# Kernel optimization log

Measured on AMD Instinct MI355X. Metric: run time of the kernel, lower is better.

## Reference

```python
import jax, jax.numpy as jnp
import numpy as np

B, T, C = 1, 4096, 1024
NH, NKV, HD = 16, 4, 64
N_REP = NH // NKV
WIN = 1024
EPS = 1e-5
ROPE_THETA = 10000.0


def setup_inputs() -> dict:
    key = jax.random.key(0)
    ks = jax.random.split(key, 6)
    s = 1.0 / np.sqrt(C)
    x = jax.random.normal(ks[0], (B, T, C), jnp.float32)
    wq = jax.random.normal(ks[1], (NH * HD, C), jnp.float32) * s
    wk = jax.random.normal(ks[2], (NKV * HD, C), jnp.float32) * s
    wv = jax.random.normal(ks[3], (NKV * HD, C), jnp.float32) * s
    wo = jax.random.normal(ks[4], (C, NH * HD), jnp.float32) * (1.0 / np.sqrt(NH * HD))
    q_norm_w = jnp.ones((HD,), jnp.float32)
    k_norm_w = jnp.ones((HD,), jnp.float32)
    # RoPE tables: (T, HD//2)
    inv_freq = 1.0 / (ROPE_THETA ** (np.arange(0, HD, 2, dtype=np.float32) / HD))
    ang = np.outer(np.arange(T, dtype=np.float32), inv_freq)
    freqs_cos = jnp.asarray(np.cos(ang), jnp.float32)
    freqs_sin = jnp.asarray(np.sin(ang), jnp.float32)
    return {"x": x, "wq": wq, "wk": wk, "wv": wv, "wo": wo,
            "q_norm_w": q_norm_w, "k_norm_w": k_norm_w,
            "freqs_cos": freqs_cos, "freqs_sin": freqs_sin}


def _rmsnorm(v, w):
    # RMSNorm over last dim (per-head)
    return v * jax.lax.rsqrt(jnp.mean(v * v, axis=-1, keepdims=True) + EPS) * w


def _rope(v, cos, sin):
    # v: (B, T, H, HD); interleaved complex rotation, matching torch polar freqs_cis
    vr, vi = v[..., 0::2], v[..., 1::2]
    c = cos[None, :, None, :]
    s = sin[None, :, None, :]
    out_r = vr * c - vi * s
    out_i = vr * s + vi * c
    return jnp.stack([out_r, out_i], axis=-1).reshape(v.shape)


def reference(x, wq, wk, wv, wo, q_norm_w, k_norm_w, freqs_cos, freqs_sin):
    xq = jnp.einsum('btc,dc->btd', x, wq).reshape(B, T, NH, HD)
    xk = jnp.einsum('btc,dc->btd', x, wk).reshape(B, T, NKV, HD)
    xv = jnp.einsum('btc,dc->btd', x, wv).reshape(B, T, NKV, HD)
    # per-head QK RMSNorm
    xq = _rmsnorm(xq, q_norm_w)
    xk = _rmsnorm(xk, k_norm_w)
    # RoPE
    xq = _rope(xq, freqs_cos, freqs_sin)
    xk = _rope(xk, freqs_cos, freqs_sin)
    # GQA: expand kv heads
    xk = jnp.repeat(xk, N_REP, axis=2)  # (B, T, NH, HD)
    xv = jnp.repeat(xv, N_REP, axis=2)
    scale = 1.0 / np.sqrt(HD)
    scores = jnp.einsum('bthd,bshd->bhts', xq, xk) * scale
    i = jnp.arange(T)[:, None]
    j = jnp.arange(T)[None, :]
    mask = (i >= j) & (i - j < WIN)  # causal + sliding window
    scores = jnp.where(mask[None, None], scores, -jnp.inf)
    attn = jax.nn.softmax(scores, axis=-1)
    y = jnp.einsum('bhts,bshd->bthd', attn, xv).reshape(B, T, NH * HD)
    return jnp.einsum('btd,cd->btc', y, wo)
```

## Files before the change

### kernel.cpp

```cpp
#include <hip/hip_runtime.h>
#include <hip/hip_bf16.h>


#define WIN_SZ 1024

typedef __attribute__((ext_vector_type(8))) short short8;
typedef __attribute__((ext_vector_type(8))) unsigned short ushort8;
typedef __attribute__((ext_vector_type(4))) float f32x4;
typedef __attribute__((ext_vector_type(16))) float f32x16;

__device__ __forceinline__ unsigned short f2bf(float f) {
  union { float f; unsigned u; } v; v.f = f;
  unsigned r = v.u + 0x7fffu + ((v.u >> 16) & 1u);
  return (unsigned short)(r >> 16);
}

__device__ __forceinline__ float bf2f(unsigned short b) {
  union { unsigned u; float f; } v; v.u = ((unsigned)b) << 16; return v.f;
}

__device__ __forceinline__ unsigned pk2bf(float lo, float hi) {
  __hip_bfloat162 h = __float22bfloat162_rn(make_float2(lo, hi));
  union { __hip_bfloat162 h; unsigned u; } c; c.h = h; return c.u;
}

__device__ __forceinline__ short8 frag4(unsigned w0, unsigned w1, unsigned w2, unsigned w3) {
  union { unsigned u[4]; short8 s; } x;
  x.u[0] = w0; x.u[1] = w1; x.u[2] = w2; x.u[3] = w3; return x.s;
}

__device__ __forceinline__ ushort8 pack8(float4 a, float4 b) {
  union { unsigned u[4]; ushort8 s; } x;
  x.u[0] = pk2bf(a.x, a.y); x.u[1] = pk2bf(a.z, a.w);
  x.u[2] = pk2bf(b.x, b.y); x.u[3] = pk2bf(b.z, b.w);
  return x.s;
}

__global__ __launch_bounds__(256) void k_gemm_qkv(const float* __restrict__ x,
                                                  const float* __restrict__ wq,
                                                  const float* __restrict__ wk,
                                                  const float* __restrict__ wv,
                                                  unsigned short* __restrict__ C) {
  __shared__ unsigned short As[128 * 64];
  __shared__ unsigned short Bs[128 * 64];
  char* Asb = (char*)As;
  char* Bsb = (char*)Bs;
  const int tid = threadIdx.x;
  const int w = tid >> 6, l = tid & 63;
  const int wr = w >> 1, wc = w & 1;
  const int r = l & 15, g = l >> 4;
  const int m0 = blockIdx.y * 128, n0 = blockIdx.x * 128;
  const int crow = tid >> 3, cslot = tid & 7;

  const float* Bp;
  if (n0 < 1024) Bp = wq + (size_t)n0 * 1024;
  else if (n0 < 1280) Bp = wk + (size_t)(n0 - 1024) * 1024;
  else Bp = wv + (size_t)(n0 - 1280) * 1024;

  f32x4 acc[4][4];
#pragma unroll
  for (int i = 0; i < 4; i++)
#pragma unroll
    for (int j = 0; j < 4; j++) acc[i][j] = {0.f, 0.f, 0.f, 0.f};

  for (int k0 = 0; k0 < 1024; k0 += 64) {
#pragma unroll
    for (int i = 0; i < 4; i++) {
      int row = crow + i * 32;
      int dst = row * 128 + ((cslot * 16) ^ ((row & 7) << 4));
      const float4* ap = (const float4*)(x + (size_t)(m0 + row) * 1024 + k0 + cslot * 8);
      *(ushort8*)(Asb + dst) = pack8(ap[0], ap[1]);
      const float4* bp = (const float4*)(Bp + (size_t)row * 1024 + k0 + cslot * 8);
      *(ushort8*)(Bsb + dst) = pack8(bp[0], bp[1]);
    }
    __syncthreads();
#pragma unroll
    for (int kk = 0; kk < 2; kk++) {
      short8 af[4], bfr[4];
#pragma unroll
      for (int mi = 0; mi < 4; mi++) {
        int row = wr * 64 + mi * 16 + r;
        af[mi] = *(const short8*)(Asb + row * 128 + ((kk * 64 + g * 16) ^ ((row & 7) << 4)));
      }
#pragma unroll
      for (int nj = 0; nj < 4; nj++) {
        int row = wc * 64 + nj * 16 + r;
        bfr[nj] = *(const short8*)(Bsb + row * 128 + ((kk * 64 + g * 16) ^ ((row & 7) << 4)));
      }
#pragma unroll
      for (int mi = 0; mi < 4; mi++)
#pragma unroll
        for (int nj = 0; nj < 4; nj++)
          acc[mi][nj] = __builtin_amdgcn_mfma_f32_16x16x32_bf16(af[mi], bfr[nj], acc[mi][nj], 0, 0, 0);
    }
    __syncthreads();
  }

#pragma unroll
  for (int mi = 0; mi < 4; mi++)
#pragma unroll
    for (int nj = 0; nj < 4; nj++) {
      int row = m0 + wr * 64 + mi * 16 + g * 4;
      int col = n0 + wc * 64 + nj * 16 + r;
#pragma unroll
      for (int e = 0; e < 4; e++)
        C[(size_t)(row + e) * 1536 + col] = f2bf(acc[mi][nj][e]);
    }
}

__global__ __launch_bounds__(256) void k_gemm_out(const unsigned short* __restrict__ A,
                                                  const float* __restrict__ wo,
                                                  float* __restrict__ C) {
  __shared__ unsigned short As[128 * 64];
  __shared__ unsigned short Bs[128 * 64];
  char* Asb = (char*)As;
  char* Bsb = (char*)Bs;
  const int tid = threadIdx.x;
  const int w = tid >> 6, l = tid & 63;
  const int wr = w >> 1, wc = w & 1;
  const int r = l & 15, g = l >> 4;
  const int m0 = blockIdx.y * 128, n0 = blockIdx.x * 128;
  const int crow = tid >> 3, cslot = tid & 7;

  f32x4 acc[4][4];
#pragma unroll
  for (int i = 0; i < 4; i++)
#pragma unroll
    for (int j = 0; j < 4; j++) acc[i][j] = {0.f, 0.f, 0.f, 0.f};

  for (int k0 = 0; k0 < 1024; k0 += 64) {
#pragma unroll
    for (int i = 0; i < 4; i++) {
      int row = crow + i * 32;
      int dst = row * 128 + ((cslot * 16) ^ ((row & 7) << 4));
      ushort8 va = *(const ushort8*)(A + (size_t)(m0 + row) * 1024 + k0 + cslot * 8);
      *(ushort8*)(Asb + dst) = va;
      const float4* bp = (const float4*)(wo + (size_t)(n0 + row) * 1024 + k0 + cslot * 8);
      *(ushort8*)(Bsb + dst) = pack8(bp[0], bp[1]);
    }
    __syncthreads();
#pragma unroll
    for (int kk = 0; kk < 2; kk++) {
      short8 af[4], bfr[4];
#pragma unroll
      for (int mi = 0; mi < 4; mi++) {
        int row = wr * 64 + mi * 16 + r;
        af[mi] = *(const short8*)(Asb + row * 128 + ((kk * 64 + g * 16) ^ ((row & 7) << 4)));
      }
#pragma unroll
      for (int nj = 0; nj < 4; nj++) {
        int row = wc * 64 + nj * 16 + r;
        bfr[nj] = *(const short8*)(Bsb + row * 128 + ((kk * 64 + g * 16) ^ ((row & 7) << 4)));
      }
#pragma unroll
      for (int mi = 0; mi < 4; mi++)
#pragma unroll
        for (int nj = 0; nj < 4; nj++)
          acc[mi][nj] = __builtin_amdgcn_mfma_f32_16x16x32_bf16(af[mi], bfr[nj], acc[mi][nj], 0, 0, 0);
    }
    __syncthreads();
  }

#pragma unroll
  for (int mi = 0; mi < 4; mi++)
#pragma unroll
    for (int nj = 0; nj < 4; nj++) {
      int row = m0 + wr * 64 + mi * 16 + g * 4;
      int col = n0 + wc * 64 + nj * 16 + r;
#pragma unroll
      for (int e = 0; e < 4; e++)
        C[(size_t)(row + e) * 1024 + col] = acc[mi][nj][e];
    }
}

__global__ __launch_bounds__(256) void k_normrope(const unsigned short* __restrict__ QKV,
                                                  const float* __restrict__ qw,
                                                  const float* __restrict__ kw,
                                                  const float* __restrict__ fc,
                                                  const float* __restrict__ fs,
                                                  unsigned short* __restrict__ Qb,
                                                  unsigned short* __restrict__ Kb,
                                                  unsigned short* __restrict__ Vtg) {
  int gid = blockIdx.x * 4 + (threadIdx.x >> 6);
  int l = threadIdx.x & 63;
  int t = gid / 24;
  int u = gid - t * 24;
  if (u < 16) {
    float v = bf2f(QKV[(size_t)t * 1536 + u * 64 + l]);
    float ss = v * v;
#pragma unroll
    for (int off = 32; off; off >>= 1) ss += __shfl_xor(ss, off);
    float rms = rsqrtf(ss * (1.0f / 64.0f) + 1e-5f);
    float vn = v * rms * qw[l];
    float c = fc[t * 32 + (l >> 1)], s = fs[t * 32 + (l >> 1)];
    float p = __shfl_xor(vn, 1);
    float out = (l & 1) ? (p * s + vn * c) : (vn * c - p * s);
    Qb[(size_t)t * 1024 + u * 64 + l] = f2bf(out * 0.1803368801111204f);
  } else if (u < 20) {
    int hh = u - 16;
    float v = bf2f(QKV[(size_t)t * 1536 + 1024 + hh * 64 + l]);
    float ss = v * v;
#pragma unroll
    for (int off = 32; off; off >>= 1) ss += __shfl_xor(ss, off);
    float rms = rsqrtf(ss * (1.0f / 64.0f) + 1e-5f);
    float vn = v * rms * kw[l];
    float c = fc[t * 32 + (l >> 1)], s = fs[t * 32 + (l >> 1)];
    float p = __shfl_xor(vn, 1);
    float out = (l & 1) ? (p * s + vn * c) : (vn * c - p * s);
    Kb[(size_t)t * 256 + hh * 64 + l] = f2bf(out);
  } else {
    int hh = u - 20;
    Vtg[(size_t)(hh * 64 + l) * 4096 + t] = QKV[(size_t)t * 1536 + 1280 + hh * 64 + l];
  }
}

__global__ __launch_bounds__(512, 4) void k_attn4(const unsigned short* __restrict__ Qb,
                                                  const unsigned short* __restrict__ Kb,
                                                  const unsigned short* __restrict__ Vtg,
                                                  unsigned short* __restrict__ Yb) {
  __shared__ char smem[4 * 8192 + 1024];
  char* stage = smem;
  float* Obuf = (float*)smem;
  float* ml = (float*)(smem + 32768);

  const int hk = blockIdx.y;
  const int q0 = blockIdx.x * 32;
  const int tid = threadIdx.x, w = tid >> 6, l = tid & 63;
  const int hh = w & 3, half = w >> 2;
  const int h = hk * 4 + hh;
  const int l31 = l & 31, hi = l >> 5, l15 = l & 15;
  const int qrow = q0 + l31;

  int jlo = q0 - (WIN_SZ - 1);
  if (jlo < 0) jlo = 0;
  jlo &= ~63;
  const int jlast = ((q0 + 31) >> 6) << 6;
  const int nt = ((jlast - jlo) >> 6) + 1;
  const int nh0 = (nt + 1) >> 1;

  const int sb = tid >> 7;
  const int su = tid & 127;
  const int srow = su >> 1;
  const int sg = (su & 1) * 4;
  const int sbase = sb * 8192 + (srow & 31) * 256;
  const int srx = (srow & 15) << 4;
  const int srh = (srow >> 5) * 128;
  const bool isV = sb & 1;
  const unsigned short* gK = Kb + (size_t)srow * 256 + hk * 64 + sg * 8;
  const unsigned short* gV = Vtg + (size_t)(hk * 64 + srow) * 4096 + sg * 8;

  short8 qf[4];
#pragma unroll
  for (int ks = 0; ks < 4; ks++)
    qf[ks] = *(const short8*)(Qb + (size_t)qrow * 1024 + h * 64 + ks * 16 + hi * 8);

  f32x16 accO0, accO1;
#pragma unroll
  for (int i = 0; i < 16; i++) { accO0[i] = 0.f; accO1[i] = 0.f; }
  float m = -1e30f, lsum = 0.f;

  ushort8 pre[4];
  auto prefetch = [&](int s) {
    int jt0 = jlo + (s << 6);
    int t1 = nh0 + s;
    int jt1 = (t1 < nt) ? (jlo + (t1 << 6)) : jlo;
    int jt = (sb >= 2) ? jt1 : jt0;
    if (!isV) {
      const unsigned short* g = gK + (size_t)jt * 256;
#pragma unroll
      for (int e = 0; e < 4; e++) pre[e] = *(const ushort8*)(g + e * 8);
    } else {
      const unsigned short* g = gV + jt;
#pragma unroll
      for (int e = 0; e < 4; e++) pre[e] = *(const ushort8*)(g + e * 8);
    }
  };
  prefetch(0);

  const int kbase = half * 16384;
  const int vbase = kbase + 8192;

  for (int s = 0; s < nh0; ++s) {
    __syncthreads();
#pragma unroll
    for (int e = 0; e < 4; e++) {
      int dst = sbase + ((srh + (sg + e) * 16) ^ srx);
      *(ushort8*)(stage + dst) = pre[e];
    }
    __syncthreads();
    if (s + 1 < nh0) prefetch(s + 1);

    const int myt = half ? (nh0 + s) : s;
    if (myt < nt) {
      const int jt = jlo + (myt << 6);

      f32x16 st0, st1;
#pragma unroll
      for (int i = 0; i < 16; i++) { st0[i] = 0.f; st1[i] = 0.f; }
      __builtin_amdgcn_s_setprio(1);
#pragma unroll
      for (int ks = 0; ks < 4; ks++) {
        int colb = ks * 32 + hi * 16;
        short8 kf0 = *(const short8*)(stage + kbase + l31 * 256 + (colb ^ (l15 << 4)));
        st0 = __builtin_amdgcn_mfma_f32_32x32x16_bf16(kf0, qf[ks], st0, 0, 0, 0);
        short8 kf1 = *(const short8*)(stage + kbase + l31 * 256 + ((128 + colb) ^ (l15 << 4)));
        st1 = __builtin_amdgcn_mfma_f32_32x32x16_bf16(kf1, qf[ks], st1, 0, 0, 0);
      }
      __builtin_amdgcn_s_setprio(0);

      if (jt + 63 > q0 || (q0 + 31) - jt >= WIN_SZ) {
        const int jb = jt + hi * 4;
#pragma unroll
        for (int rg = 0; rg < 16; rg++) {
          int j0 = jb + (rg & 3) + 8 * (rg >> 2);
          if (!((j0 <= qrow) && (qrow - j0 < WIN_SZ))) st0[rg] = -3.0e38f;
          int j1 = j0 + 32;
          if (!((j1 <= qrow) && (qrow - j1 < WIN_SZ))) st1[rg] = -3.0e38f;
        }
      }

      float mx = st0[0];
#pragma unroll
      for (int rg = 1; rg < 16; rg++) mx = fmaxf(mx, st0[rg]);
#pragma unroll
      for (int rg = 0; rg < 16; rg++) mx = fmaxf(mx, st1[rg]);
      mx = fmaxf(mx, __shfl_xor(mx, 32));
      if (!__all(mx <= m + 8.0f)) {
        float mnew = fmaxf(m, mx);
        float alpha = exp2f(m - mnew);
#pragma unroll
        for (int rg = 0; rg < 16; rg++) { accO0[rg] *= alpha; accO1[rg] *= alpha; }
        lsum *= alpha;
        m = mnew;
      }
      float ps = 0.f;
#pragma unroll
      for (int rg = 0; rg < 16; rg++) { st0[rg] = exp2f(st0[rg] - m); ps += st0[rg]; }
#pragma unroll
      for (int rg = 0; rg < 16; rg++) { st1[rg] = exp2f(st1[rg] - m); ps += st1[rg]; }
      lsum += ps;

      unsigned pd0[2][4], pd1[2][4];
#pragma unroll
      for (int b = 0; b < 4; b++) {
        pd0[0][b] = pk2bf(st0[4 * b], st0[4 * b + 1]);
        pd1[0][b] = pk2bf(st0[4 * b + 2], st0[4 * b + 3]);
        pd0[1][b] = pk2bf(st1[4 * b], st1[4 * b + 1]);
        pd1[1][b] = pk2bf(st1[4 * b + 2], st1[4 * b + 3]);
      }

      __builtin_amdgcn_s_setprio(1);
#pragma unroll
      for (int jj = 0; jj < 2; jj++) {
#pragma unroll
        for (int ks2 = 0; ks2 < 2; ks2++) {
          unsigned a0 = pd0[jj][2 * ks2], a1 = pd0[jj][2 * ks2 + 1];
          unsigned b0 = pd1[jj][2 * ks2], b1 = pd1[jj][2 * ks2 + 1];
          unsigned a0x = __shfl_xor(a0, 32), a1x = __shfl_xor(a1, 32);
          unsigned b0x = __shfl_xor(b0, 32), b1x = __shfl_xor(b1, 32);
          unsigned w0 = hi ? a1x : a0;
          unsigned w1 = hi ? b1x : b0;
          unsigned w2 = hi ? a1 : a0x;
          unsigned w3 = hi ? b1 : b0x;
          short8 pf = frag4(w0, w1, w2, w3);
          int colb2 = jj * 64 + ks2 * 32 + hi * 16;
          short8 vf0 = *(const short8*)(stage + vbase + l31 * 256 + (colb2 ^ (l15 << 4)));
          accO0 = __builtin_amdgcn_mfma_f32_32x32x16_bf16(vf0, pf, accO0, 0, 0, 0);
          short8 vf1 = *(const short8*)(stage + vbase + l31 * 256 + ((128 + colb2) ^ (l15 << 4)));
          accO1 = __builtin_amdgcn_mfma_f32_32x32x16_bf16(vf1, pf, accO1, 0, 0, 0);
        }
      }
      __builtin_amdgcn_s_setprio(0);
    }
  }

  lsum += __shfl_xor(lsum, 32);
  __syncthreads();
  if (half == 1) {
#pragma unroll
    for (int dd = 0; dd < 2; dd++) {
      const f32x16& a = dd ? accO1 : accO0;
#pragma unroll
      for (int rg = 0; rg < 16; rg++) {
        int d = dd * 32 + 8 * (rg >> 2) + 4 * hi + (rg & 3);
        Obuf[(hh * 64 + d) * 32 + l31] = a[rg];
      }
    }
    if (!hi) { ml[(hh * 2 + 0) * 32 + l31] = m; ml[(hh * 2 + 1) * 32 + l31] = lsum; }
  }
  __syncthreads();
  if (half == 0) {
    float m1 = ml[(hh * 2 + 0) * 32 + l31];
    float l1 = ml[(hh * 2 + 1) * 32 + l31];
    float ms = fmaxf(m, m1);
    float a0 = exp2f(m - ms), a1 = exp2f(m1 - ms);
    float inv = 1.0f / (lsum * a0 + l1 * a1);
    a0 *= inv; a1 *= inv;
#pragma unroll
    for (int dd = 0; dd < 2; dd++) {
      const f32x16& a = dd ? accO1 : accO0;
#pragma unroll
      for (int b = 0; b < 4; b++) {
        float o[4];
#pragma unroll
        for (int e = 0; e < 4; e++) {
          int d = dd * 32 + 8 * b + 4 * hi + e;
          o[e] = a[4 * b + e] * a0 + Obuf[(hh * 64 + d) * 32 + l31] * a1;
        }
        union { unsigned u[2]; ushort4 v; } ov;
        ov.u[0] = pk2bf(o[0], o[1]);
        ov.u[1] = pk2bf(o[2], o[3]);
        *(ushort4*)(Yb + (size_t)qrow * 1024 + h * 64 + dd * 32 + b * 8 + hi * 4) = ov.v;
      }
    }
  }
}

extern "C" void kernel_launch(void* const* d_in, const int* in_sizes, int n_in,
                              void* d_out, int out_size, void* d_ws, size_t ws_size,
                              hipStream_t stream) {
  const float* x = (const float*)d_in[0];
  const float* wq = (const float*)d_in[1];
  const float* wk = (const float*)d_in[2];
  const float* wv = (const float*)d_in[3];
  const float* wo = (const float*)d_in[4];
  const float* qw = (const float*)d_in[5];
  const float* kw = (const float*)d_in[6];
  const float* fc = (const float*)d_in[7];
  const float* fs = (const float*)d_in[8];
  float* out = (float*)d_out;

  char* p = (char*)d_ws;
  auto alloc = [&](size_t b) {
    char* q = p;
    p += (b + 255) & ~(size_t)255;
    return q;
  };
  unsigned short* QKVb = (unsigned short*)alloc((size_t)4096 * 1536 * 2);
  unsigned short* Qb = (unsigned short*)alloc((size_t)4096 * 1024 * 2);
  unsigned short* Kb = (unsigned short*)alloc((size_t)4096 * 256 * 2);
  unsigned short* Vtg = (unsigned short*)alloc((size_t)256 * 4096 * 2);
  unsigned short* Yb = (unsigned short*)alloc((size_t)4096 * 1024 * 2);

  k_gemm_qkv<<<dim3(12, 32), 256, 0, stream>>>(x, wq, wk, wv, QKVb);
  k_normrope<<<24576, 256, 0, stream>>>(QKVb, qw, kw, fc, fs, Qb, Kb, Vtg);
  k_attn4<<<dim3(128, 4), 512, 0, stream>>>(Qb, Kb, Vtg, Yb);
  k_gemm_out<<<dim3(8, 32), 256, 0, stream>>>(Yb, wo, out);
}
```

Before: 130.8 us.

## Pre-convert inputs to bf16 and use direct global-to-LDS loads in GEMMs

Adds a single kernel that converts x and all weight matrices from fp32 to bf16 up front. The two GEMMs are merged into one templated kernel that streams bf16 tiles straight into LDS with global_load_lds, replacing per-tile fp32 loads and in-register conversion. This removes redundant conversion work and halves GEMM operand traffic, but adds an extra launch and a full write and read of the converted tensors. The LDS XOR swizzle is dropped, which may bring back bank conflicts on fragment reads.

```diff
diff --git a/kernel.cpp b/kernel.cpp
--- a/kernel.cpp
+++ b/kernel.cpp
@@ -9,6 +9,11 @@
 typedef __attribute__((ext_vector_type(4))) float f32x4;
 typedef __attribute__((ext_vector_type(16))) float f32x16;
 
+#define GLOAD_LDS16(g, s)                                              \
+  __builtin_amdgcn_global_load_lds(                                    \
+      (const __attribute__((address_space(1))) unsigned int*)(g),      \
+      (__attribute__((address_space(3))) unsigned int*)(s), 16, 0, 0)
+
 __device__ __forceinline__ unsigned short f2bf(float f) {
   union { float f; unsigned u; } v; v.f = f;
   unsigned r = v.u + 0x7fffu + ((v.u >> 16) & 1u);
@@ -29,33 +34,43 @@
   x.u[0] = w0; x.u[1] = w1; x.u[2] = w2; x.u[3] = w3; return x.s;
 }
 
-__device__ __forceinline__ ushort8 pack8(float4 a, float4 b) {
-  union { unsigned u[4]; ushort8 s; } x;
-  x.u[0] = pk2bf(a.x, a.y); x.u[1] = pk2bf(a.z, a.w);
-  x.u[2] = pk2bf(b.x, b.y); x.u[3] = pk2bf(b.z, b.w);
-  return x.s;
-}
-
-__global__ __launch_bounds__(256) void k_gemm_qkv(const float* __restrict__ x,
-                                                  const float* __restrict__ wq,
-                                                  const float* __restrict__ wk,
-                                                  const float* __restrict__ wv,
-                                                  unsigned short* __restrict__ C) {
+__global__ __launch_bounds__(256) void k_f2b_all(const float* __restrict__ x,
+                                                 const float* __restrict__ wq,
+                                                 const float* __restrict__ wk,
+                                                 const float* __restrict__ wv,
+                                                 const float* __restrict__ wo,
+                                                 unsigned short* __restrict__ xb,
+                                                 unsigned short* __restrict__ wqkvb,
+                                                 unsigned short* __restrict__ wob) {
+  int q = blockIdx.x * 256 + threadIdx.x;
+  const float* src;
+  unsigned short* dst;
+  int off;
+  if (q < 1048576) { src = x; dst = xb; off = q; }
+  else if (q < 1310720) { src = wq; dst = wqkvb; off = q - 1048576; }
+  else if (q < 1376256) { src = wk; dst = wqkvb + 1024 * 1024; off = q - 1310720; }
+  else if (q < 1441792) { src = wv; dst = wqkvb + 1280 * 1024; off = q - 1376256; }
+  else { src = wo; dst = wob; off = q - 1441792; }
+  float4 v = ((const float4*)src)[off];
+  ushort4 o;
+  o.x = f2bf(v.x); o.y = f2bf(v.y); o.z = f2bf(v.z); o.w = f2bf(v.w);
+  ((ushort4*)dst)[off] = o;
+}
+
+template <int BF16OUT>
+__global__ __launch_bounds__(256) void k_gemm16(const unsigned short* __restrict__ A,
+                                                const unsigned short* __restrict__ B,
+                                                void* __restrict__ Cv,
+                                                int M, int N, int K) {
   __shared__ unsigned short As[128 * 64];
   __shared__ unsigned short Bs[128 * 64];
-  char* Asb = (char*)As;
-  char* Bsb = (char*)Bs;
   const int tid = threadIdx.x;
   const int w = tid >> 6, l = tid & 63;
   const int wr = w >> 1, wc = w & 1;
   const int r = l & 15, g = l >> 4;
   const int m0 = blockIdx.y * 128, n0 = blockIdx.x * 128;
-  const int crow = tid >> 3, cslot = tid & 7;
-
-  const float* Bp;
-  if (n0 < 1024) Bp = wq + (size_t)n0 * 1024;
-  else if (n0 < 1280) Bp = wk + (size_t)(n0 - 1024) * 1024;
-  else Bp = wv + (size_t)(n0 - 1280) * 1024;
+  const int lr = l >> 3, lc = l & 7;
+  const int srowb = w * 32;
 
   f32x4 acc[4][4];
 #pragma unroll
@@ -63,30 +78,25 @@
 #pragma unroll
     for (int j = 0; j < 4; j++) acc[i][j] = {0.f, 0.f, 0.f, 0.f};
 
-  for (int k0 = 0; k0 < 1024; k0 += 64) {
-#pragma unroll
-    for (int i = 0; i < 4; i++) {
-      int row = crow + i * 32;
-      int dst = row * 128 + ((cslot * 16) ^ ((row & 7) << 4));
-      const float4* ap = (const float4*)(x + (size_t)(m0 + row) * 1024 + k0 + cslot * 8);
-      *(ushort8*)(Asb + dst) = pack8(ap[0], ap[1]);
-      const float4* bp = (const float4*)(Bp + (size_t)row * 1024 + k0 + cslot * 8);
-      *(ushort8*)(Bsb + dst) = pack8(bp[0], bp[1]);
+  const unsigned short* Ag = A + (size_t)(m0 + srowb + lr) * K + lc * 8;
+  const unsigned short* Bg = B + (size_t)(n0 + srowb + lr) * K + lc * 8;
+
+  for (int k0 = 0; k0 < K; k0 += 64) {
+#pragma unroll
+    for (int it = 0; it < 4; it++) {
+      GLOAD_LDS16(Ag + (size_t)(it * 8) * K + k0, As + (srowb + it * 8) * 64);
+      GLOAD_LDS16(Bg + (size_t)(it * 8) * K + k0, Bs + (srowb + it * 8) * 64);
     }
     __syncthreads();
 #pragma unroll
     for (int kk = 0; kk < 2; kk++) {
       short8 af[4], bfr[4];
 #pragma unroll
-      for (int mi = 0; mi < 4; mi++) {
-        int row = wr * 64 + mi * 16 + r;
-        af[mi] = *(const short8*)(Asb + row * 128 + ((kk * 64 + g * 16) ^ ((row & 7) << 4)));
-      }
-#pragma unroll
-      for (int nj = 0; nj < 4; nj++) {
-        int row = wc * 64 + nj * 16 + r;
-        bfr[nj] = *(const short8*)(Bsb + row * 128 + ((kk * 64 + g * 16) ^ ((row & 7) << 4)));
-      }
+      for (int mi = 0; mi < 4; mi++)
+        af[mi] = *(const short8*)((const char*)As + (wr * 64 + mi * 16 + r) * 128 + kk * 64 + g * 16);
+#pragma unroll
+      for (int nj = 0; nj < 4; nj++)
+        bfr[nj] = *(const short8*)((const char*)Bs + (wc * 64 + nj * 16 + r) * 128 + kk * 64 + g * 16);
 #pragma unroll
       for (int mi = 0; mi < 4; mi++)
 #pragma unroll
@@ -102,74 +112,17 @@
     for (int nj = 0; nj < 4; nj++) {
       int row = m0 + wr * 64 + mi * 16 + g * 4;
       int col = n0 + wc * 64 + nj * 16 + r;
-#pragma unroll
-      for (int e = 0; e < 4; e++)
-        C[(size_t)(row + e) * 1536 + col] = f2bf(acc[mi][nj][e]);
-    }
-}
-
-__global__ __launch_bounds__(256) void k_gemm_out(const unsigned short* __restrict__ A,
-                                                  const float* __restrict__ wo,
-                                                  float* __restrict__ C) {
-  __shared__ unsigned short As[128 * 64];
-  __shared__ unsigned short Bs[128 * 64];
-  char* Asb = (char*)As;
-  char* Bsb = (char*)Bs;
-  const int tid = threadIdx.x;
-  const int w = tid >> 6, l = tid & 63;
-  const int wr = w >> 1, wc = w & 1;
-  const int r = l & 15, g = l >> 4;
-  const int m0 = blockIdx.y * 128, n0 = blockIdx.x * 128;
-  const int crow = tid >> 3, cslot = tid & 7;
-
-  f32x4 acc[4][4];
-#pragma unroll
-  for (int i = 0; i < 4; i++)
-#pragma unroll
-    for (int j = 0; j < 4; j++) acc[i][j] = {0.f, 0.f, 0.f, 0.f};
-
-  for (int k0 = 0; k0 < 1024; k0 += 64) {
-#pragma unroll
-    for (int i = 0; i < 4; i++) {
-      int row = crow + i * 32;
-      int dst = row * 128 + ((cslot * 16) ^ ((row & 7) << 4));
-      ushort8 va = *(const ushort8*)(A + (size_t)(m0 + row) * 1024 + k0 + cslot * 8);
-      *(ushort8*)(Asb + dst) = va;
-      const float4* bp = (const float4*)(wo + (size_t)(n0 + row) * 1024 + k0 + cslot * 8);
-      *(ushort8*)(Bsb + dst) = pack8(bp[0], bp[1]);
-    }
-    __syncthreads();
-#pragma unroll
-    for (int kk = 0; kk < 2; kk++) {
-      short8 af[4], bfr[4];
-#pragma unroll
-      for (int mi = 0; mi < 4; mi++) {
-        int row = wr * 64 + mi * 16 + r;
-        af[mi] = *(const short8*)(Asb + row * 128 + ((kk * 64 + g * 16) ^ ((row & 7) << 4)));
-      }
-#pragma unroll
-      for (int nj = 0; nj < 4; nj++) {
-        int row = wc * 64 + nj * 16 + r;
-        bfr[nj] = *(const short8*)(Bsb + row * 128 + ((kk * 64 + g * 16) ^ ((row & 7) << 4)));
-      }
-#pragma unroll
-      for (int mi = 0; mi < 4; mi++)
-#pragma unroll
-        for (int nj = 0; nj < 4; nj++)
-          acc[mi][nj] = __builtin_amdgcn_mfma_f32_16x16x32_bf16(af[mi], bfr[nj], acc[mi][nj], 0, 0, 0);
-    }
-    __syncthreads();
-  }
-
-#pragma unroll
-  for (int mi = 0; mi < 4; mi++)
-#pragma unroll
-    for (int nj = 0; nj < 4; nj++) {
-      int row = m0 + wr * 64 + mi * 16 + g * 4;
-      int col = n0 + wc * 64 + nj * 16 + r;
-#pragma unroll
-      for (int e = 0; e < 4; e++)
-        C[(size_t)(row + e) * 1024 + col] = acc[mi][nj][e];
+      if (BF16OUT) {
+        unsigned short* C = (unsigned short*)Cv;
+#pragma unroll
+        for (int e = 0; e < 4; e++)
+          C[(size_t)(row + e) * N + col] = f2bf(acc[mi][nj][e]);
+      } else {
+        float* C = (float*)Cv;
+#pragma unroll
+        for (int e = 0; e < 4; e++)
+          C[(size_t)(row + e) * N + col] = acc[mi][nj][e];
+      }
     }
 }
 
@@ -436,14 +389,18 @@
     p += (b + 255) & ~(size_t)255;
     return q;
   };
+  unsigned short* xb = (unsigned short*)alloc((size_t)4096 * 1024 * 2);
+  unsigned short* wqkvb = (unsigned short*)alloc((size_t)1536 * 1024 * 2);
+  unsigned short* wob = (unsigned short*)alloc((size_t)1024 * 1024 * 2);
   unsigned short* QKVb = (unsigned short*)alloc((size_t)4096 * 1536 * 2);
   unsigned short* Qb = (unsigned short*)alloc((size_t)4096 * 1024 * 2);
   unsigned short* Kb = (unsigned short*)alloc((size_t)4096 * 256 * 2);
   unsigned short* Vtg = (unsigned short*)alloc((size_t)256 * 4096 * 2);
   unsigned short* Yb = (unsigned short*)alloc((size_t)4096 * 1024 * 2);
 
-  k_gemm_qkv<<<dim3(12, 32), 256, 0, stream>>>(x, wq, wk, wv, QKVb);
+  k_f2b_all<<<6656, 256, 0, stream>>>(x, wq, wk, wv, wo, xb, wqkvb, wob);
+  k_gemm16<1><<<dim3(12, 32), 256, 0, stream>>>(xb, wqkvb, QKVb, 4096, 1536, 1024);
   k_normrope<<<24576, 256, 0, stream>>>(QKVb, qw, kw, fc, fs, Qb, Kb, Vtg);
   k_attn4<<<dim3(128, 4), 512, 0, stream>>>(Qb, Kb, Vtg, Yb);
-  k_gemm_out<<<dim3(8, 32), 256, 0, stream>>>(Yb, wo, out);
-}
+  k_gemm16<0><<<dim3(8, 32), 256, 0, stream>>>(Yb, wob, out, 4096, 1024, 1024);
+}
```

Measured after the change: 124.0 us. 1.05x faster.
